# Performance work log

Hardware: AMD Instinct MI355X
Metric: run time of the kernel (lower is better)

## Reference

```python
import jax, jax.numpy as jnp
import numpy as np

N = 50000      # total nodes after flattening [1,1,N,D]
E = 600000     # random edges (plus N self-loops appended)
D = 128        # in_dim == out_dim
H = 8          # num_heads
DP = D // H    # per-head dim (each_out_dim)
SLOPE = 0.2    # DGL GATv2Conv default negative_slope


def setup_inputs() -> dict:
    key = jax.random.key(0)
    ks = jax.random.split(key, 6)
    x = jax.random.normal(ks[0], (1, 1, N, D), dtype=jnp.float32)
    s = 1.0 / np.sqrt(D).astype(np.float32)
    # GATv2Conv params: separate src/dst linear projections (share_weights=False),
    # with bias, plus a per-head attention vector.
    w_src = jax.random.uniform(ks[1], (D, H * DP), jnp.float32, -s, s)
    b_src = jnp.zeros((H * DP,), jnp.float32)
    w_dst = jax.random.uniform(ks[2], (D, H * DP), jnp.float32, -s, s)
    b_dst = jnp.zeros((H * DP,), jnp.float32)
    attn_w = jax.random.uniform(ks[3], (H, DP), jnp.float32, -s, s)
    self_loop = jnp.arange(N, dtype=jnp.int32)
    src = jnp.concatenate([jax.random.randint(ks[4], (E,), 0, N, dtype=jnp.int32), self_loop])
    dst = jnp.concatenate([jax.random.randint(ks[5], (E,), 0, N, dtype=jnp.int32), self_loop])
    return {"x": x, "w_src": w_src, "b_src": b_src, "w_dst": w_dst,
            "b_dst": b_dst, "attn_w": attn_w, "src": src, "dst": dst}


def reference(x, w_src, b_src, w_dst, b_dst, attn_w, src, dst):
    shape = x.shape
    h = x.reshape(-1, shape[3])                       # (N, D)
    n = h.shape[0]
    fs = (h @ w_src + b_src).reshape(n, H, DP)        # (N, H, Dp) source proj
    fd = (h @ w_dst + b_dst).reshape(n, H, DP)        # (N, H, Dp) dest proj
    # GATv2: e_ij = a^T LeakyReLU(W_s h_i + W_d h_j)
    e = jax.nn.leaky_relu(fs[src] + fd[dst], SLOPE)   # (E, H, Dp)
    logits = jnp.einsum('ehd,hd->eh', e, attn_w)      # (E, H)
    # segment softmax over incoming edges of each destination node
    m = jax.ops.segment_max(logits, dst, num_segments=n)
    m = jnp.where(jnp.isfinite(m), m, 0.0)
    ex = jnp.exp(logits - m[dst])                     # (E, H)
    denom = jax.ops.segment_sum(ex, dst, num_segments=n)
    alpha = ex / denom[dst]                           # (E, H)
    # weighted scatter-add aggregation of source features
    out = jax.ops.segment_sum(alpha[:, :, None] * fs[src], dst, num_segments=n)
    return out.reshape(shape)
```

## Files before the change

### kernel.cpp

```cpp
#include <hip/hip_runtime.h>
#include <hip/hip_bf16.h>

#define HH 8
#define DP 16
#define DD 128
#define SLOPE 0.2f

#define BM 32
__global__ __launch_bounds__(256) void proj_count_kernel(
    const float* __restrict__ x,
    const float* __restrict__ w_src, const float* __restrict__ b_src,
    const float* __restrict__ w_dst, const float* __restrict__ b_dst,
    float* __restrict__ fs, float* __restrict__ fd, int n,
    const int* __restrict__ dst, int* __restrict__ count, int ecount) {
  __shared__ float xs[BM][DD];
  const int tid = threadIdx.x;
  const int block0 = blockIdx.x * BM;

  for (int i = tid; i < BM * DD / 4; i += 256) {
    int m = i >> 5;
    int k = (i & 31) << 2;
    int node = block0 + m;
    float4 v = make_float4(0.f, 0.f, 0.f, 0.f);
    if (node < n) v = *reinterpret_cast<const float4*>(x + (size_t)node * DD + k);
    *reinterpret_cast<float4*>(&xs[m][k]) = v;
  }
  __syncthreads();

  const int c = tid & (DD - 1);
  const int m0 = (tid >> 7) * 16;

  float acc_s[16], acc_d[16];
#pragma unroll
  for (int m = 0; m < 16; ++m) { acc_s[m] = 0.f; acc_d[m] = 0.f; }

  float ws0 = w_src[0 * DD + c], ws1 = w_src[1 * DD + c];
  float ws2 = w_src[2 * DD + c], ws3 = w_src[3 * DD + c];
  float wd0 = w_dst[0 * DD + c], wd1 = w_dst[1 * DD + c];
  float wd2 = w_dst[2 * DD + c], wd3 = w_dst[3 * DD + c];

  for (int k = 0; k < DD; k += 4) {
    const int kn = (k + 4) & (DD - 1);
    float nws0 = w_src[(kn + 0) * DD + c], nws1 = w_src[(kn + 1) * DD + c];
    float nws2 = w_src[(kn + 2) * DD + c], nws3 = w_src[(kn + 3) * DD + c];
    float nwd0 = w_dst[(kn + 0) * DD + c], nwd1 = w_dst[(kn + 1) * DD + c];
    float nwd2 = w_dst[(kn + 2) * DD + c], nwd3 = w_dst[(kn + 3) * DD + c];
#pragma unroll
    for (int m = 0; m < 16; ++m) {
      float4 xv = *reinterpret_cast<const float4*>(&xs[m0 + m][k]);
      acc_s[m] = fmaf(xv.x, ws0, acc_s[m]);
      acc_s[m] = fmaf(xv.y, ws1, acc_s[m]);
      acc_s[m] = fmaf(xv.z, ws2, acc_s[m]);
      acc_s[m] = fmaf(xv.w, ws3, acc_s[m]);
      acc_d[m] = fmaf(xv.x, wd0, acc_d[m]);
      acc_d[m] = fmaf(xv.y, wd1, acc_d[m]);
      acc_d[m] = fmaf(xv.z, wd2, acc_d[m]);
      acc_d[m] = fmaf(xv.w, wd3, acc_d[m]);
    }
    ws0 = nws0; ws1 = nws1; ws2 = nws2; ws3 = nws3;
    wd0 = nwd0; wd1 = nwd1; wd2 = nwd2; wd3 = nwd3;
  }

  const float bs = b_src[c];
  const float bd = b_dst[c];
#pragma unroll
  for (int m = 0; m < 16; ++m) {
    int node = block0 + m0 + m;
    if (node < n) {
      fs[(size_t)node * DD + c] = acc_s[m] + bs;
      fd[(size_t)node * DD + c] = acc_d[m] + bd;
    }
  }

  const int nblocks = (n + BM - 1) / BM;
  const int stride = nblocks * 256;
  for (int e = blockIdx.x * 256 + tid; e < ecount; e += stride)
    atomicAdd(&count[dst[e]], 1);
}

__global__ __launch_bounds__(256) void alloc_kernel(const int* __restrict__ count,
                                                    int* __restrict__ cursor,
                                                    int* __restrict__ total, int n) {
  const int lane = threadIdx.x & 63;
  const int wid = threadIdx.x >> 6;
  const int wave = blockIdx.x * 4 + wid;
  const int i0 = wave * 256;

  int excl[4];
  int carry = 0;
#pragma unroll
  for (int j = 0; j < 4; ++j) {
    int i = i0 + j * 64 + lane;
    int v = (i < n) ? count[i] : 0;
    int incl = v;
#pragma unroll
    for (int off = 1; off < 64; off <<= 1) {
      int t = __shfl_up(incl, (unsigned)off, 64);
      if (lane >= off) incl += t;
    }
    excl[j] = carry + incl - v;
    carry += __shfl(incl, 63, 64);
  }
  int base = 0;
  if (lane == 63) base = atomicAdd(total, carry);
  base = __shfl(base, 63, 64);
#pragma unroll
  for (int j = 0; j < 4; ++j) {
    int i = i0 + j * 64 + lane;
    if (i < n) cursor[i] = base + excl[j];
  }
}

__global__ __launch_bounds__(256) void scatter_kernel(const int* __restrict__ src,
                                                      const int* __restrict__ dst,
                                                      int* __restrict__ cursor,
                                                      int* __restrict__ edge_src, int ecount) {
  int e = blockIdx.x * 256 + threadIdx.x;
  if (e < ecount) {
    int pos = atomicAdd(&cursor[dst[e]], 1);
    edge_src[pos] = src[e];
  }
}

__global__ __launch_bounds__(256) void node_kernel(const float* __restrict__ fs,
                                                   const float* __restrict__ fd,
                                                   const float* __restrict__ attn_w,
                                                   const int* __restrict__ cursor,
                                                   const int* __restrict__ count,
                                                   const int* __restrict__ edge_src,
                                                   float* __restrict__ out, int n) {
  const int wid = threadIdx.x >> 6;
  const int lane = threadIdx.x & 63;
  const int node = blockIdx.x * 4 + wid;
  if (node >= n) return;

  const int d0 = lane * 2;
  const float2 aw = *reinterpret_cast<const float2*>(&attn_w[d0]);
  const float2 fdv = *reinterpret_cast<const float2*>(&fd[(size_t)node * DD + d0]);

  const int e1 = cursor[node];
  const int e0 = e1 - count[node];

  float mx[4] = {-1e30f, -1e30f, -1e30f, -1e30f};
  float den[4] = {0.f, 0.f, 0.f, 0.f};
  float2 ac[4] = {{0.f, 0.f}, {0.f, 0.f}, {0.f, 0.f}, {0.f, 0.f}};

  auto logit_of = [&](float2 fsv) -> float {
    float t0 = fsv.x + fdv.x; t0 = (t0 > 0.f) ? t0 : t0 * SLOPE;
    float t1 = fsv.y + fdv.y; t1 = (t1 > 0.f) ? t1 : t1 * SLOPE;
    float p = aw.x * t0 + aw.y * t1;
    p += __shfl_xor(p, 1, 64);
    p += __shfl_xor(p, 2, 64);
    p += __shfl_xor(p, 4, 64);
    return p;
  };
  auto upd = [](float& m, float& dn, float2& a, float logit, float2 fsv) {
    float mn = fmaxf(m, logit);
    float sc = __expf(m - mn);
    float p = __expf(logit - mn);
    dn = dn * sc + p;
    a.x = a.x * sc + p * fsv.x;
    a.y = a.y * sc + p * fsv.y;
    m = mn;
  };
  auto gather = [&](int s) -> float2 {
    return *reinterpret_cast<const float2*>(&fs[(size_t)s * DD + d0]);
  };

  int e = e0;
  const int nfull = (e1 - e0) >> 2;
  if (nfull > 0) {
    float2 f0 = gather(edge_src[e0]);
    float2 f1 = gather(edge_src[e0 + 1]);
    float2 f2 = gather(edge_src[e0 + 2]);
    float2 f3 = gather(edge_src[e0 + 3]);
    for (int g = 1; g < nfull; ++g) {
      const int b = e0 + g * 4;
      float2 g0 = gather(edge_src[b]);
      float2 g1 = gather(edge_src[b + 1]);
      float2 g2 = gather(edge_src[b + 2]);
      float2 g3 = gather(edge_src[b + 3]);
      float l0 = logit_of(f0), l1 = logit_of(f1);
      float l2 = logit_of(f2), l3 = logit_of(f3);
      upd(mx[0], den[0], ac[0], l0, f0);
      upd(mx[1], den[1], ac[1], l1, f1);
      upd(mx[2], den[2], ac[2], l2, f2);
      upd(mx[3], den[3], ac[3], l3, f3);
      f0 = g0; f1 = g1; f2 = g2; f3 = g3;
    }
    float l0 = logit_of(f0), l1 = logit_of(f1);
    float l2 = logit_of(f2), l3 = logit_of(f3);
    upd(mx[0], den[0], ac[0], l0, f0);
    upd(mx[1], den[1], ac[1], l1, f1);
    upd(mx[2], den[2], ac[2], l2, f2);
    upd(mx[3], den[3], ac[3], l3, f3);
    e = e0 + nfull * 4;
  }
  for (; e < e1; ++e) {
    float2 f0 = gather(edge_src[e]);
    float l0 = logit_of(f0);
    upd(mx[0], den[0], ac[0], l0, f0);
  }

  float M = fmaxf(fmaxf(mx[0], mx[1]), fmaxf(mx[2], mx[3]));
  float denom = 0.f, ax = 0.f, ay = 0.f;
#pragma unroll
  for (int j = 0; j < 4; ++j) {
    float s = __expf(mx[j] - M);
    denom += den[j] * s;
    ax += ac[j].x * s;
    ay += ac[j].y * s;
  }

  float inv = (denom > 0.f) ? 1.f / denom : 0.f;
  *reinterpret_cast<float2*>(&out[(size_t)node * DD + d0]) =
      make_float2(ax * inv, ay * inv);
}

extern "C" void kernel_launch(void* const* d_in, const int* in_sizes, int n_in,
                              void* d_out, int out_size, void* d_ws, size_t ws_size,
                              hipStream_t stream) {
  const float* x      = (const float*)d_in[0];
  const float* w_src  = (const float*)d_in[1];
  const float* b_src  = (const float*)d_in[2];
  const float* w_dst  = (const float*)d_in[3];
  const float* b_dst  = (const float*)d_in[4];
  const float* attn_w = (const float*)d_in[5];
  const int* src = (const int*)d_in[6];
  const int* dst = (const int*)d_in[7];
  float* out = (float*)d_out;

  const int n = in_sizes[0] / DD;
  const int ecount = in_sizes[6];

  size_t off = 0;
  float* fs = (float*)((char*)d_ws + off); off += (size_t)n * DD * sizeof(float);
  float* fd = (float*)((char*)d_ws + off); off += (size_t)n * DD * sizeof(float);
  int* edge_src = (int*)((char*)d_ws + off); off += (size_t)ecount * sizeof(int);
  int* cursor   = (int*)((char*)d_ws + off); off += (size_t)n * sizeof(int);
  int* count    = (int*)((char*)d_ws + off); off += (size_t)n * sizeof(int);
  int* total    = (int*)((char*)d_ws + off); off += sizeof(int);
  (void)ws_size;

  hipMemsetAsync(count, 0, (size_t)(n + 1) * sizeof(int), stream);

  const int proj_blocks = (n + BM - 1) / BM;
  proj_count_kernel<<<proj_blocks, 256, 0, stream>>>(
      x, w_src, b_src, w_dst, b_dst, fs, fd, n, dst, count, ecount);
  alloc_kernel<<<(n + 1023) / 1024, 256, 0, stream>>>(count, cursor, total, n);
  scatter_kernel<<<(ecount + 255) / 256, 256, 0, stream>>>(src, dst, cursor, edge_src, ecount);
  node_kernel<<<(n + 3) / 4, 256, 0, stream>>>(fs, fd, attn_w, cursor, count, edge_src, out, n);
}
```

Measured before the change: 253.7 us.

## Keep projection weight column in registers and prefetch edge indices in node kernel

The projection kernel now assigns half the threads to the source projection and half to the destination projection. Each thread keeps its full 128-entry weight column in registers and processes 64-node tiles from shared memory. The node aggregation kernel makes its edge range wave-uniform with readfirstlane and software-pipelines the edge_src index loads one group ahead of the feature gathers. The aim is to cut repeated weight loads and gather latency, at the cost of high register pressure and fewer accumulators per thread.

```diff
diff --git a/kernel.cpp b/kernel.cpp
--- a/kernel.cpp
+++ b/kernel.cpp
@@ -6,74 +6,74 @@
 #define DD 128
 #define SLOPE 0.2f
 
-#define BM 32
+#define BN 64
 __global__ __launch_bounds__(256) void proj_count_kernel(
     const float* __restrict__ x,
     const float* __restrict__ w_src, const float* __restrict__ b_src,
     const float* __restrict__ w_dst, const float* __restrict__ b_dst,
     float* __restrict__ fs, float* __restrict__ fd, int n,
     const int* __restrict__ dst, int* __restrict__ count, int ecount) {
-  __shared__ float xs[BM][DD];
+  __shared__ float xs[BN][DD];
   const int tid = threadIdx.x;
-  const int block0 = blockIdx.x * BM;
-
-  for (int i = tid; i < BM * DD / 4; i += 256) {
-    int m = i >> 5;
-    int k = (i & 31) << 2;
-    int node = block0 + m;
-    float4 v = make_float4(0.f, 0.f, 0.f, 0.f);
-    if (node < n) v = *reinterpret_cast<const float4*>(x + (size_t)node * DD + k);
-    *reinterpret_cast<float4*>(&xs[m][k]) = v;
-  }
-  __syncthreads();
-
   const int c = tid & (DD - 1);
-  const int m0 = (tid >> 7) * 16;
-
-  float acc_s[16], acc_d[16];
-#pragma unroll
-  for (int m = 0; m < 16; ++m) { acc_s[m] = 0.f; acc_d[m] = 0.f; }
-
-  float ws0 = w_src[0 * DD + c], ws1 = w_src[1 * DD + c];
-  float ws2 = w_src[2 * DD + c], ws3 = w_src[3 * DD + c];
-  float wd0 = w_dst[0 * DD + c], wd1 = w_dst[1 * DD + c];
-  float wd2 = w_dst[2 * DD + c], wd3 = w_dst[3 * DD + c];
-
-  for (int k = 0; k < DD; k += 4) {
-    const int kn = (k + 4) & (DD - 1);
-    float nws0 = w_src[(kn + 0) * DD + c], nws1 = w_src[(kn + 1) * DD + c];
-    float nws2 = w_src[(kn + 2) * DD + c], nws3 = w_src[(kn + 3) * DD + c];
-    float nwd0 = w_dst[(kn + 0) * DD + c], nwd1 = w_dst[(kn + 1) * DD + c];
-    float nwd2 = w_dst[(kn + 2) * DD + c], nwd3 = w_dst[(kn + 3) * DD + c];
-#pragma unroll
-    for (int m = 0; m < 16; ++m) {
-      float4 xv = *reinterpret_cast<const float4*>(&xs[m0 + m][k]);
-      acc_s[m] = fmaf(xv.x, ws0, acc_s[m]);
-      acc_s[m] = fmaf(xv.y, ws1, acc_s[m]);
-      acc_s[m] = fmaf(xv.z, ws2, acc_s[m]);
-      acc_s[m] = fmaf(xv.w, ws3, acc_s[m]);
-      acc_d[m] = fmaf(xv.x, wd0, acc_d[m]);
-      acc_d[m] = fmaf(xv.y, wd1, acc_d[m]);
-      acc_d[m] = fmaf(xv.z, wd2, acc_d[m]);
-      acc_d[m] = fmaf(xv.w, wd3, acc_d[m]);
-    }
-    ws0 = nws0; ws1 = nws1; ws2 = nws2; ws3 = nws3;
-    wd0 = nwd0; wd1 = nwd1; wd2 = nwd2; wd3 = nwd3;
-  }
-
-  const float bs = b_src[c];
-  const float bd = b_dst[c];
-#pragma unroll
-  for (int m = 0; m < 16; ++m) {
-    int node = block0 + m0 + m;
-    if (node < n) {
-      fs[(size_t)node * DD + c] = acc_s[m] + bs;
-      fd[(size_t)node * DD + c] = acc_d[m] + bd;
-    }
-  }
-
-  const int nblocks = (n + BM - 1) / BM;
-  const int stride = nblocks * 256;
+  const bool is_src = tid < DD;
+
+  const float* __restrict__ w = is_src ? w_src : w_dst;
+  float* __restrict__ outp = is_src ? fs : fd;
+  const float bias = is_src ? b_src[c] : b_dst[c];
+
+  float wreg[DD];
+#pragma unroll
+  for (int k = 0; k < DD; ++k) wreg[k] = w[k * DD + c];
+
+  const int ntiles = (n + BN - 1) / BN;
+  for (int t = blockIdx.x; t < ntiles; t += gridDim.x) {
+    const int node0 = t * BN;
+    __syncthreads();
+    for (int i = tid; i < BN * DD / 4; i += 256) {
+      int m = i >> 5;
+      int k = (i & 31) << 2;
+      int node = node0 + m;
+      float4 v = make_float4(0.f, 0.f, 0.f, 0.f);
+      if (node < n) v = *reinterpret_cast<const float4*>(x + (size_t)node * DD + k);
+      *reinterpret_cast<float4*>(&xs[m][k]) = v;
+    }
+    __syncthreads();
+
+    for (int m = 0; m < BN; m += 4) {
+      float a0 = 0.f, a1 = 0.f, a2 = 0.f, a3 = 0.f;
+#pragma unroll
+      for (int k = 0; k < DD; k += 4) {
+        float4 x0 = *reinterpret_cast<const float4*>(&xs[m + 0][k]);
+        float4 x1 = *reinterpret_cast<const float4*>(&xs[m + 1][k]);
+        float4 x2 = *reinterpret_cast<const float4*>(&xs[m + 2][k]);
+        float4 x3 = *reinterpret_cast<const float4*>(&xs[m + 3][k]);
+        a0 = fmaf(x0.x, wreg[k], a0);
+        a0 = fmaf(x0.y, wreg[k + 1], a0);
+        a0 = fmaf(x0.z, wreg[k + 2], a0);
+        a0 = fmaf(x0.w, wreg[k + 3], a0);
+        a1 = fmaf(x1.x, wreg[k], a1);
+        a1 = fmaf(x1.y, wreg[k + 1], a1);
+        a1 = fmaf(x1.z, wreg[k + 2], a1);
+        a1 = fmaf(x1.w, wreg[k + 3], a1);
+        a2 = fmaf(x2.x, wreg[k], a2);
+        a2 = fmaf(x2.y, wreg[k + 1], a2);
+        a2 = fmaf(x2.z, wreg[k + 2], a2);
+        a2 = fmaf(x2.w, wreg[k + 3], a2);
+        a3 = fmaf(x3.x, wreg[k], a3);
+        a3 = fmaf(x3.y, wreg[k + 1], a3);
+        a3 = fmaf(x3.z, wreg[k + 2], a3);
+        a3 = fmaf(x3.w, wreg[k + 3], a3);
+      }
+      const int node = node0 + m;
+      if (node + 0 < n) outp[(size_t)(node + 0) * DD + c] = a0 + bias;
+      if (node + 1 < n) outp[(size_t)(node + 1) * DD + c] = a1 + bias;
+      if (node + 2 < n) outp[(size_t)(node + 2) * DD + c] = a2 + bias;
+      if (node + 3 < n) outp[(size_t)(node + 3) * DD + c] = a3 + bias;
+    }
+  }
+
+  const int stride = gridDim.x * 256;
   for (int e = blockIdx.x * 256 + tid; e < ecount; e += stride)
     atomicAdd(&count[dst[e]], 1);
 }
@@ -138,8 +138,8 @@
   const float2 aw = *reinterpret_cast<const float2*>(&attn_w[d0]);
   const float2 fdv = *reinterpret_cast<const float2*>(&fd[(size_t)node * DD + d0]);
 
-  const int e1 = cursor[node];
-  const int e0 = e1 - count[node];
+  const int e1 = __builtin_amdgcn_readfirstlane(cursor[node]);
+  const int e0 = e1 - __builtin_amdgcn_readfirstlane(count[node]);
 
   float mx[4] = {-1e30f, -1e30f, -1e30f, -1e30f};
   float den[4] = {0.f, 0.f, 0.f, 0.f};
@@ -170,23 +170,26 @@
   int e = e0;
   const int nfull = (e1 - e0) >> 2;
   if (nfull > 0) {
-    float2 f0 = gather(edge_src[e0]);
-    float2 f1 = gather(edge_src[e0 + 1]);
-    float2 f2 = gather(edge_src[e0 + 2]);
-    float2 f3 = gather(edge_src[e0 + 3]);
+    int i0 = edge_src[e0], i1 = edge_src[e0 + 1];
+    int i2 = edge_src[e0 + 2], i3 = edge_src[e0 + 3];
+    float2 f0 = gather(i0), f1 = gather(i1), f2 = gather(i2), f3 = gather(i3);
+    int b = (1 < nfull) ? e0 + 4 : e0;
+    int j0 = edge_src[b], j1 = edge_src[b + 1];
+    int j2 = edge_src[b + 2], j3 = edge_src[b + 3];
+
     for (int g = 1; g < nfull; ++g) {
-      const int b = e0 + g * 4;
-      float2 g0 = gather(edge_src[b]);
-      float2 g1 = gather(edge_src[b + 1]);
-      float2 g2 = gather(edge_src[b + 2]);
-      float2 g3 = gather(edge_src[b + 3]);
+      float2 h0 = gather(j0), h1 = gather(j1), h2 = gather(j2), h3 = gather(j3);
+      int b2 = (g + 1 < nfull) ? e0 + (g + 1) * 4 : e0;
+      int k0 = edge_src[b2], k1 = edge_src[b2 + 1];
+      int k2 = edge_src[b2 + 2], k3 = edge_src[b2 + 3];
       float l0 = logit_of(f0), l1 = logit_of(f1);
       float l2 = logit_of(f2), l3 = logit_of(f3);
       upd(mx[0], den[0], ac[0], l0, f0);
       upd(mx[1], den[1], ac[1], l1, f1);
       upd(mx[2], den[2], ac[2], l2, f2);
       upd(mx[3], den[3], ac[3], l3, f3);
-      f0 = g0; f1 = g1; f2 = g2; f3 = g3;
+      f0 = h0; f1 = h1; f2 = h2; f3 = h3;
+      j0 = k0; j1 = k1; j2 = k2; j3 = k3;
     }
     float l0 = logit_of(f0), l1 = logit_of(f1);
     float l2 = logit_of(f2), l3 = logit_of(f3);
@@ -244,8 +247,8 @@
 
   hipMemsetAsync(count, 0, (size_t)(n + 1) * sizeof(int), stream);
 
-  const int proj_blocks = (n + BM - 1) / BM;
-  proj_count_kernel<<<proj_blocks, 256, 0, stream>>>(
+  const int ntiles = (n + BN - 1) / BN;
+  proj_count_kernel<<<ntiles, 256, 0, stream>>>(
       x, w_src, b_src, w_dst, b_dst, fs, fd, n, dst, count, ecount);
   alloc_kernel<<<(n + 1023) / 1024, 256, 0, stream>>>(count, cursor, total, n);
   scatter_kernel<<<(ecount + 255) / 256, 256, 0, stream>>>(src, dst, cursor, edge_src, ecount);
```

Result: slower. 892.9 us (+252.0%).
